# Performance work log

Measured on AMD Instinct MI355X. Metric: run time of the kernel, lower is better.

Reference implementation:

```python
import jax, jax.numpy as jnp
import numpy as np

N = 50000        # nodes
E = 800000       # edges (before self-loops)
F_IN = 128       # num_features
HID = 32         # hidden_size per head
HEADS = 4
CLS = 40         # num_classes
NEG_SLOPE = 0.2  # PyG GATConv default leaky_relu slope


def setup_inputs() -> dict:
    key = jax.random.key(0)
    ks = jax.random.split(key, 10)
    s = lambda k, sh: (jax.random.normal(k, sh, jnp.float32) * 0.05)
    x = jax.random.normal(ks[0], (N, F_IN), jnp.float32)
    edge_index = jax.random.randint(ks[1], (2, E), 0, N, dtype=jnp.int64)
    W1 = s(ks[2], (F_IN, HEADS * HID))
    att_src1 = s(ks[3], (HEADS, HID))
    att_dst1 = s(ks[4], (HEADS, HID))
    b1 = jnp.zeros((HEADS * HID,), jnp.float32)
    W2 = s(ks[5], (HEADS * HID, CLS))
    att_src2 = s(ks[6], (1, CLS))
    att_dst2 = s(ks[7], (1, CLS))
    b2 = jnp.zeros((CLS,), jnp.float32)
    return {"x": x, "edge_index": edge_index, "W1": W1, "att_src1": att_src1,
            "att_dst1": att_dst1, "b1": b1, "W2": W2, "att_src2": att_src2,
            "att_dst2": att_dst2, "b2": b2}


def _add_self_loops(edge_index, num_nodes):
    ar = jnp.arange(num_nodes, dtype=edge_index.dtype)
    loops = jnp.stack([ar, ar])
    return jnp.concatenate([edge_index, loops], axis=1)


def _gat_conv(x, edge_index, W, a_src, a_dst, bias, heads, concat):
    """PyG GATConv (eval mode, additive attention, self-loops already added)."""
    n = x.shape[0]
    src, dst = edge_index[0], edge_index[1]
    h = (x @ W).reshape(n, heads, -1)                 # [N, H, C]
    a_s = jnp.einsum('nhc,hc->nh', h, a_src)          # [N, H]
    a_d = jnp.einsum('nhc,hc->nh', h, a_dst)          # [N, H]
    e = jax.nn.leaky_relu(a_s[src] + a_d[dst], NEG_SLOPE)   # [E', H]
    m = jax.ops.segment_max(e, dst, num_segments=n)   # segment softmax over dst
    ex = jnp.exp(e - m[dst])
    den = jax.ops.segment_sum(ex, dst, num_segments=n)
    alpha = ex / den[dst]                             # [E', H]
    out = jax.ops.segment_sum(h[src] * alpha[:, :, None], dst, num_segments=n)
    out = out.reshape(n, -1) if concat else out.mean(axis=1)
    return out + bias


def reference(x, edge_index, W1, att_src1, att_dst1, b1, W2, att_src2, att_dst2, b2):
    ei = _add_self_loops(edge_index, x.shape[0])
    # dropout p=0 in eval -> identity
    h = jax.nn.relu(_gat_conv(x, ei, W1, att_src1, att_dst1, b1, HEADS, True))
    out = _gat_conv(h, ei, W2, att_src2, att_dst2, b2, 1, True)  # heads=1
    return out
```

## Files before the change

### kernel.cpp

```cpp
#include <hip/hip_runtime.h>
#include <cstdint>

#define NODES 50000
#define FIN   128
#define C1    128
#define HEADS 4
#define HID   32
#define CLS   40
#define SLOPE 0.2f

#define NBUCK ((NODES + 255) >> 8)
#define EPB 2048
#define BCAP 8192

__device__ __forceinline__ float lrelu(float v) { return v > 0.f ? v : SLOPE * v; }

__device__ __forceinline__ unsigned short f2bf(float f) {
    union { float f; unsigned u; } v; v.f = f;
    unsigned u = v.u;
    return (unsigned short)((u + 0x7FFFu + ((u >> 16) & 1u)) >> 16);
}
__device__ __forceinline__ float bf2f(unsigned short b) {
    union { unsigned u; float f; } v; v.u = ((unsigned)b) << 16;
    return v.f;
}
__device__ __forceinline__ float bflo(unsigned u) {
    union { unsigned x; float f; } v; v.x = u << 16; return v.f;
}
__device__ __forceinline__ float bfhi(unsigned u) {
    union { unsigned x; float f; } v; v.x = u & 0xffff0000u; return v.f;
}
__device__ __forceinline__ unsigned cvtpk(float a, float b) {
    unsigned r;
    asm("v_cvt_pk_bf16_f32 %0, %1, %2" : "=v"(r) : "v"(a), "v"(b));
    return r;
}

typedef __attribute__((ext_vector_type(8))) short bf16x8;
typedef __attribute__((ext_vector_type(4))) float f32x4;
typedef __attribute__((ext_vector_type(4), aligned(4))) int int4a;
typedef __attribute__((ext_vector_type(2), aligned(4))) int int2a;

__device__ __forceinline__ void acc8(float w, uint4 p, float* ac) {
    ac[0] = fmaf(w, bflo(p.x), ac[0]); ac[1] = fmaf(w, bfhi(p.x), ac[1]);
    ac[2] = fmaf(w, bflo(p.y), ac[2]); ac[3] = fmaf(w, bfhi(p.y), ac[3]);
    ac[4] = fmaf(w, bflo(p.z), ac[4]); ac[5] = fmaf(w, bfhi(p.z), ac[5]);
    ac[6] = fmaf(w, bflo(p.w), ac[6]); ac[7] = fmaf(w, bfhi(p.w), ac[7]);
}

__global__ __launch_bounds__(256) void k_prep(const float* __restrict__ W1,
                                              const float* __restrict__ W2,
                                              unsigned short* __restrict__ w1t,
                                              unsigned short* __restrict__ w2t,
                                              int* __restrict__ bwp) {
    const int b = blockIdx.x, t = threadIdx.x;
    if (b < 8) {
        __shared__ unsigned short Tb[16][136];
        const int n0 = b * 16;
        const int k = t & 127, g = t >> 7;
#pragma unroll
        for (int i = 0; i < 8; i++)
            Tb[g * 8 + i][k] = f2bf(W1[(size_t)k * C1 + n0 + g * 8 + i]);
        __syncthreads();
        {
            int nl = t >> 4, k8 = (t & 15) * 8;
            *(uint4*)(w1t + (n0 + nl) * 128 + k8) = *(uint4*)(&Tb[nl][k8]);
        }
    } else {
        for (int p = t; p < CLS * 128; p += 256) {
            int n = p >> 7, k = p & 127;
            w2t[n * 128 + k] = f2bf(W2[(size_t)k * CLS + n]);
        }
        if (t < NBUCK) bwp[t] = t * BCAP;
    }
}

__global__ __launch_bounds__(256) void k_front(const float* __restrict__ X,
                                               const unsigned short* __restrict__ w1t,
                                               const float* __restrict__ AS,
                                               const float* __restrict__ AD,
                                               unsigned short* __restrict__ h1b,
                                               float* __restrict__ as1,
                                               float* __restrict__ ad1,
                                               const int* __restrict__ src,
                                               const int* __restrict__ dst, int E,
                                               int* __restrict__ bwp,
                                               int* __restrict__ tmp, int GB1) {
    __shared__ unsigned short Asm[64][136];
    __shared__ unsigned short Wt[128][136];
    __shared__ int cnt[NBUCK];
    __shared__ int bbs[NBUCK];
    const int t = threadIdx.x;

    if (blockIdx.x >= GB1) {
        for (int i = t; i < NBUCK; i += 256) cnt[i] = 0;
        __syncthreads();
        const int e0 = (blockIdx.x - GB1) * EPB;
        int v[8], rb[8];
#pragma unroll
        for (int k = 0; k < 8; k++) {
            int e = e0 + k * 256 + t;
            rb[k] = -1;
            if (e < E) {
                int d = dst[e], s = src[e];
                int b = d >> 8;
                int r = atomicAdd(&cnt[b], 1);
                v[k] = (s << 8) | (d & 255);
                rb[k] = (r << 8) | b;
            }
        }
        __syncthreads();
        for (int i = t; i < NBUCK; i += 256) {
            int c = cnt[i];
            bbs[i] = c ? atomicAdd(&bwp[i], c) : 0;
        }
        __syncthreads();
#pragma unroll
        for (int k = 0; k < 8; k++) {
            if (rb[k] >= 0) {
                int b = rb[k] & 255;
                int r = rb[k] >> 8;
                tmp[bbs[b] + r] = v[k];
            }
        }
        return;
    }

    const int row0 = blockIdx.x * 64;
#pragma unroll
    for (int i = 0; i < 8; i++) {
        int p = i * 256 + t;
        int n = p >> 4, k8 = (p & 15) * 8;
        *(uint4*)(&Wt[n][k8]) = *(const uint4*)(w1t + n * 128 + k8);
    }
    {
        int r = t >> 2, c0 = (t & 3) * 32;
        int gr = row0 + r;
        if (gr < NODES) {
#pragma unroll
            for (int i = 0; i < 4; i++) {
                float4 va = *(const float4*)(X + (size_t)gr * FIN + c0 + i * 8);
                float4 vb = *(const float4*)(X + (size_t)gr * FIN + c0 + i * 8 + 4);
                uint4 pk;
                pk.x = cvtpk(va.x, va.y);
                pk.y = cvtpk(va.z, va.w);
                pk.z = cvtpk(vb.x, vb.y);
                pk.w = cvtpk(vb.z, vb.w);
                *(uint4*)(&Asm[r][c0 + i * 8]) = pk;
            }
        } else {
            uint4 z = make_uint4(0, 0, 0, 0);
#pragma unroll
            for (int i = 0; i < 4; i++) *(uint4*)(&Asm[r][c0 + i * 8]) = z;
        }
    }
    __syncthreads();

    const int w = t >> 6, l = t & 63;
    const int lm = l & 15, quad = l >> 4;
    f32x4 acc[8];
#pragma unroll
    for (int ct = 0; ct < 8; ct++) acc[ct] = (f32x4){0.f, 0.f, 0.f, 0.f};
#pragma unroll
    for (int kt = 0; kt < 4; kt++) {
        bf16x8 a = *(const bf16x8*)(&Asm[w * 16 + lm][kt * 32 + quad * 8]);
#pragma unroll
        for (int ct = 0; ct < 8; ct++) {
            bf16x8 b = *(const bf16x8*)(&Wt[ct * 16 + lm][kt * 32 + quad * 8]);
            acc[ct] = __builtin_amdgcn_mfma_f32_16x16x32_bf16(a, b, acc[ct], 0, 0, 0);
        }
    }
    __syncthreads();
#pragma unroll
    for (int ct = 0; ct < 8; ct++)
#pragma unroll
        for (int r = 0; r < 4; r++)
            Asm[w * 16 + quad * 4 + r][ct * 16 + lm] = f2bf(acc[ct][r]);
    __syncthreads();
    {
        int r = t >> 2, c0 = (t & 3) * 32;
        int gr = row0 + r;
        if (gr < NODES) {
#pragma unroll
            for (int i = 0; i < 4; i++)
                *(uint4*)(h1b + (size_t)gr * C1 + c0 + i * 8) =
                    *(uint4*)(&Asm[r][c0 + i * 8]);
        }
    }
    {
        int r = t >> 2, h = t & 3;
        int gr = row0 + r;
        if (gr < NODES) {
            float s = 0.f, d = 0.f;
#pragma unroll
            for (int i = 0; i < 4; i++) {
                uint4 hv = *(const uint4*)(&Asm[r][h * 32 + i * 8]);
                float4 a0 = *(const float4*)(AS + h * HID + i * 8);
                float4 a1 = *(const float4*)(AS + h * HID + i * 8 + 4);
                float4 d0 = *(const float4*)(AD + h * HID + i * 8);
                float4 d1 = *(const float4*)(AD + h * HID + i * 8 + 4);
                float v0 = bflo(hv.x), v1 = bfhi(hv.x), v2 = bflo(hv.y), v3 = bfhi(hv.y);
                float v4 = bflo(hv.z), v5 = bfhi(hv.z), v6 = bflo(hv.w), v7 = bfhi(hv.w);
                s = fmaf(v0, a0.x, s); s = fmaf(v1, a0.y, s);
                s = fmaf(v2, a0.z, s); s = fmaf(v3, a0.w, s);
                s = fmaf(v4, a1.x, s); s = fmaf(v5, a1.y, s);
                s = fmaf(v6, a1.z, s); s = fmaf(v7, a1.w, s);
                d = fmaf(v0, d0.x, d); d = fmaf(v1, d0.y, d);
                d = fmaf(v2, d0.z, d); d = fmaf(v3, d0.w, d);
                d = fmaf(v4, d1.x, d); d = fmaf(v5, d1.y, d);
                d = fmaf(v6, d1.z, d); d = fmaf(v7, d1.w, d);
            }
            as1[gr * HEADS + h] = s;
            ad1[gr * HEADS + h] = d;
        }
    }
}

__global__ __launch_bounds__(512) void k_bucketB(const int* __restrict__ bwp,
                                                 const int* __restrict__ tmp,
                                                 int* __restrict__ col,
                                                 int* __restrict__ rowptr,
                                                 int* __restrict__ degarr) {
    __shared__ int degs[256];
    __shared__ int wp[256];
    __shared__ int wsum[4];
    const int b = blockIdx.x, t = threadIdx.x;
    const int n0 = b << 8;
    const int beg = b * BCAP;
    const int end = bwp[b];
    if (t < 256) degs[t] = 0;
    __syncthreads();
    for (int e = beg + t; e < end; e += 512)
        atomicAdd(&degs[tmp[e] & 255], 1);
    __syncthreads();
    int d = 0, incl = 0;
    const int lane = t & 63, w = t >> 6;
    if (t < 256) {
        d = degs[t];
        incl = d;
#pragma unroll
        for (int s = 1; s < 64; s <<= 1) {
            int u = __shfl_up(incl, s);
            if (lane >= s) incl += u;
        }
        if (lane == 63) wsum[w] = incl;
    }
    __syncthreads();
    if (t == 0) {
        int r = 0;
#pragma unroll
        for (int i = 0; i < 4; i++) { int x = wsum[i]; wsum[i] = r; r += x; }
    }
    __syncthreads();
    if (t < 256) {
        const int excl = incl - d + wsum[w] + beg;
        const int nidx = n0 + t;
        if (nidx < NODES) { rowptr[nidx] = excl; degarr[nidx] = d; }
        wp[t] = excl;
    }
    __syncthreads();
    for (int e = beg + t; e < end; e += 512) {
        int v = tmp[e];
        int p = atomicAdd(&wp[v & 255], 1);
        col[p] = v >> 8;
    }
}

__global__ __launch_bounds__(256) void k_agg1(const unsigned short* __restrict__ h1b,
                                              const float* __restrict__ as1,
                                              const float* __restrict__ ad1,
                                              const int* __restrict__ rowptr,
                                              const int* __restrict__ degarr,
                                              const int* __restrict__ col,
                                              const float* __restrict__ b1,
                                              unsigned short* __restrict__ out1) {
    int wid = (blockIdx.x * 256 + threadIdx.x) >> 6;
    if (wid >= NODES) return;
    const int lane = threadIdx.x & 63;
    const int q  = lane >> 4;
    const int ll = lane & 15;
    const int fh = ll >> 2;
    const int n = wid;
    const float adn = ad1[n * HEADS + fh];
    const int rs = rowptr[n];
    const int re = rs + degarr[n];
    const unsigned lo = (unsigned)(ll << 4);

    float den = 0.f;
    float ac[8];
#pragma unroll
    for (int k = 0; k < 8; k++) ac[k] = 0.f;

    int base = rs;
    for (; re - base > 16; base += 32) {
        int4a ca = *(const int4a*)(col + base + q * 4);
        int4a cb = *(const int4a*)(col + base + 16 + q * 4);
        const int ia = base + q * 4;
        const int ib = base + 16 + q * 4;
        int c0 = (ia + 0 < re) ? ca.x : n;
        int c1 = (ia + 1 < re) ? ca.y : n;
        int c2 = (ia + 2 < re) ? ca.z : n;
        int c3 = (ia + 3 < re) ? ca.w : n;
        int c4 = (ib + 0 < re) ? cb.x : n;
        int c5 = (ib + 1 < re) ? cb.y : n;
        int c6 = (ib + 2 < re) ? cb.z : n;
        int c7 = (ib + 3 < re) ? cb.w : n;
        float w0 = __expf(lrelu(as1[c0 * HEADS + fh] + adn)); if (ia + 0 >= re) w0 = 0.f;
        float w1 = __expf(lrelu(as1[c1 * HEADS + fh] + adn)); if (ia + 1 >= re) w1 = 0.f;
        float w2 = __expf(lrelu(as1[c2 * HEADS + fh] + adn)); if (ia + 2 >= re) w2 = 0.f;
        float w3 = __expf(lrelu(as1[c3 * HEADS + fh] + adn)); if (ia + 3 >= re) w3 = 0.f;
        float w4 = __expf(lrelu(as1[c4 * HEADS + fh] + adn)); if (ib + 0 >= re) w4 = 0.f;
        float w5 = __expf(lrelu(as1[c5 * HEADS + fh] + adn)); if (ib + 1 >= re) w5 = 0.f;
        float w6 = __expf(lrelu(as1[c6 * HEADS + fh] + adn)); if (ib + 2 >= re) w6 = 0.f;
        float w7 = __expf(lrelu(as1[c7 * HEADS + fh] + adn)); if (ib + 3 >= re) w7 = 0.f;
        den += ((w0 + w1) + (w2 + w3)) + ((w4 + w5) + (w6 + w7));
        uint4 p0 = *(const uint4*)((const char*)h1b + (((unsigned)c0 << 8) + lo));
        uint4 p1 = *(const uint4*)((const char*)h1b + (((unsigned)c1 << 8) + lo));
        uint4 p2 = *(const uint4*)((const char*)h1b + (((unsigned)c2 << 8) + lo));
        uint4 p3 = *(const uint4*)((const char*)h1b + (((unsigned)c3 << 8) + lo));
        uint4 p4 = *(const uint4*)((const char*)h1b + (((unsigned)c4 << 8) + lo));
        uint4 p5 = *(const uint4*)((const char*)h1b + (((unsigned)c5 << 8) + lo));
        uint4 p6 = *(const uint4*)((const char*)h1b + (((unsigned)c6 << 8) + lo));
        uint4 p7 = *(const uint4*)((const char*)h1b + (((unsigned)c7 << 8) + lo));
        acc8(w0, p0, ac); acc8(w1, p1, ac); acc8(w2, p2, ac); acc8(w3, p3, ac);
        acc8(w4, p4, ac); acc8(w5, p5, ac); acc8(w6, p6, ac); acc8(w7, p7, ac);
    }
    if (base < re) {
        int4a ca = *(const int4a*)(col + base + q * 4);
        const int ia = base + q * 4;
        int c0 = (ia + 0 < re) ? ca.x : n;
        int c1 = (ia + 1 < re) ? ca.y : n;
        int c2 = (ia + 2 < re) ? ca.z : n;
        int c3 = (ia + 3 < re) ? ca.w : n;
        float w0 = __expf(lrelu(as1[c0 * HEADS + fh] + adn)); if (ia + 0 >= re) w0 = 0.f;
        float w1 = __expf(lrelu(as1[c1 * HEADS + fh] + adn)); if (ia + 1 >= re) w1 = 0.f;
        float w2 = __expf(lrelu(as1[c2 * HEADS + fh] + adn)); if (ia + 2 >= re) w2 = 0.f;
        float w3 = __expf(lrelu(as1[c3 * HEADS + fh] + adn)); if (ia + 3 >= re) w3 = 0.f;
        den += (w0 + w1) + (w2 + w3);
        uint4 p0 = *(const uint4*)((const char*)h1b + (((unsigned)c0 << 8) + lo));
        uint4 p1 = *(const uint4*)((const char*)h1b + (((unsigned)c1 << 8) + lo));
        uint4 p2 = *(const uint4*)((const char*)h1b + (((unsigned)c2 << 8) + lo));
        uint4 p3 = *(const uint4*)((const char*)h1b + (((unsigned)c3 << 8) + lo));
        acc8(w0, p0, ac); acc8(w1, p1, ac); acc8(w2, p2, ac); acc8(w3, p3, ac);
    }
    den += __shfl_xor(den, 16);
    den += __shfl_xor(den, 32);
#pragma unroll
    for (int k = 0; k < 8; k++) {
        ac[k] += __shfl_xor(ac[k], 16);
        ac[k] += __shfl_xor(ac[k], 32);
    }
    const float wself = __expf(lrelu(as1[n * HEADS + fh] + adn));
    den += wself;
    if (q == 0) {
        unsigned offs = ((unsigned)n << 8) + lo;
        uint4 sp = *(const uint4*)((const char*)h1b + offs);
        float sv[8] = {bflo(sp.x), bfhi(sp.x), bflo(sp.y), bfhi(sp.y),
                       bflo(sp.z), bfhi(sp.z), bflo(sp.w), bfhi(sp.w)};
        float4 bv0 = *(const float4*)(b1 + ll * 8);
        float4 bv1 = *(const float4*)(b1 + ll * 8 + 4);
        float bb[8] = {bv0.x, bv0.y, bv0.z, bv0.w, bv1.x, bv1.y, bv1.z, bv1.w};
        const float inv = 1.f / den;
        float o[8];
#pragma unroll
        for (int k = 0; k < 8; k++)
            o[k] = fmaxf(fmaf(wself, sv[k], ac[k]) * inv + bb[k], 0.f);
        uint4 pk;
        pk.x = cvtpk(o[0], o[1]);
        pk.y = cvtpk(o[2], o[3]);
        pk.z = cvtpk(o[4], o[5]);
        pk.w = cvtpk(o[6], o[7]);
        *(uint4*)(out1 + (size_t)n * C1 + ll * 8) = pk;
    }
}

__global__ __launch_bounds__(256) void k_gemm2(const unsigned short* __restrict__ out1b,
                                               const unsigned short* __restrict__ w2t,
                                               const float* __restrict__ AS,
                                               const float* __restrict__ AD,
                                               unsigned short* __restrict__ h2b,
                                               float* __restrict__ as2,
                                               float* __restrict__ ad2) {
    __shared__ unsigned short Asm[64][136];
    __shared__ unsigned short Wt2[48][136];
    __shared__ float Cc[64][52];
    const int t = threadIdx.x;
    const int row0 = blockIdx.x * 64;

    for (int p = t; p < 8 * 136; p += 256) Wt2[40 + p / 136][p % 136] = 0;
    for (int p = t; p < 640; p += 256) {
        int n = p >> 4, k8 = (p & 15) * 8;
        *(uint4*)(&Wt2[n][k8]) = *(const uint4*)(w2t + n * 128 + k8);
    }
    {
        int r = t >> 2, c0 = (t & 3) * 32;
        int gr = row0 + r;
        if (gr < NODES) {
#pragma unroll
            for (int i = 0; i < 4; i++)
                *(uint4*)(&Asm[r][c0 + i * 8]) =
                    *(const uint4*)(out1b + (size_t)gr * C1 + c0 + i * 8);
        } else {
            uint4 z = make_uint4(0, 0, 0, 0);
#pragma unroll
            for (int i = 0; i < 4; i++) *(uint4*)(&Asm[r][c0 + i * 8]) = z;
        }
    }
    __syncthreads();

    const int w = t >> 6, l = t & 63;
    const int lm = l & 15, quad = l >> 4;
    f32x4 acc[3];
#pragma unroll
    for (int ct = 0; ct < 3; ct++) acc[ct] = (f32x4){0.f, 0.f, 0.f, 0.f};
#pragma unroll
    for (int kt = 0; kt < 4; kt++) {
        bf16x8 a = *(const bf16x8*)(&Asm[w * 16 + lm][kt * 32 + quad * 8]);
#pragma unroll
        for (int ct = 0; ct < 3; ct++) {
            bf16x8 b = *(const bf16x8*)(&Wt2[ct * 16 + lm][kt * 32 + quad * 8]);
            acc[ct] = __builtin_amdgcn_mfma_f32_16x16x32_bf16(a, b, acc[ct], 0, 0, 0);
        }
    }
    __syncthreads();
#pragma unroll
    for (int ct = 0; ct < 3; ct++)
#pragma unroll
        for (int r = 0; r < 4; r++)
            Cc[w * 16 + quad * 4 + r][ct * 16 + lm] = acc[ct][r];
    __syncthreads();
    {
        int r = t >> 2, c0 = (t & 3) * 10;
        int gr = row0 + r;
        if (gr < NODES) {
#pragma unroll
            for (int i = 0; i < 5; i++) {
                int c = c0 + i * 2;
                unsigned pk = cvtpk(Cc[r][c], Cc[r][c + 1]);
                *(unsigned*)(h2b + (size_t)gr * 40 + c) = pk;
            }
            float s = 0.f, d = 0.f;
#pragma unroll
            for (int j = 0; j < 10; j++) {
                float v = Cc[r][c0 + j];
                s = fmaf(v, AS[c0 + j], s);
                d = fmaf(v, AD[c0 + j], d);
            }
            s += __shfl_xor(s, 1); s += __shfl_xor(s, 2);
            d += __shfl_xor(d, 1); d += __shfl_xor(d, 2);
            if ((t & 3) == 0) { as2[gr] = s; ad2[gr] = d; }
        }
    }
}

__global__ __launch_bounds__(256) void k_agg2(const unsigned short* __restrict__ h2b,
                                              const float* __restrict__ as2,
                                              const float* __restrict__ ad2,
                                              const int* __restrict__ rowptr,
                                              const int* __restrict__ degarr,
                                              const int* __restrict__ col,
                                              const float* __restrict__ b2,
                                              float* __restrict__ out) {
    int wid = (blockIdx.x * 256 + threadIdx.x) >> 6;
    if (wid >= NODES) return;
    const int lane = threadIdx.x & 63;
    const int q8 = lane >> 3, l8 = lane & 7;
    const int n = wid;
    const float adn = ad2[n];
    const int rs = rowptr[n];
    const int re = rs + degarr[n];
    const unsigned lo = (unsigned)(l8 << 4);

    float den = 0.f;
    float ac[8];
#pragma unroll
    for (int k = 0; k < 8; k++) ac[k] = 0.f;

    int base = rs;
    for (; re - base > 16; base += 32) {
        int4a cc = *(const int4a*)(col + base + q8 * 4);
        const int i0 = base + q8 * 4;
        int c0 = (i0 + 0 < re) ? cc.x : n;
        int c1 = (i0 + 1 < re) ? cc.y : n;
        int c2 = (i0 + 2 < re) ? cc.z : n;
        int c3 = (i0 + 3 < re) ? cc.w : n;
        float w0 = __expf(lrelu(as2[c0] + adn)); if (i0 + 0 >= re) w0 = 0.f;
        float w1 = __expf(lrelu(as2[c1] + adn)); if (i0 + 1 >= re) w1 = 0.f;
        float w2 = __expf(lrelu(as2[c2] + adn)); if (i0 + 2 >= re) w2 = 0.f;
        float w3 = __expf(lrelu(as2[c3] + adn)); if (i0 + 3 >= re) w3 = 0.f;
        den += (w0 + w1) + (w2 + w3);
        if (l8 < 5) {
            uint4 p0 = *(const uint4*)((const char*)h2b + ((unsigned)c0 * 80u + lo));
            uint4 p1 = *(const uint4*)((const char*)h2b + ((unsigned)c1 * 80u + lo));
            uint4 p2 = *(const uint4*)((const char*)h2b + ((unsigned)c2 * 80u + lo));
            uint4 p3 = *(const uint4*)((const char*)h2b + ((unsigned)c3 * 80u + lo));
            acc8(w0, p0, ac); acc8(w1, p1, ac);
            acc8(w2, p2, ac); acc8(w3, p3, ac);
        }
    }
    if (base < re) {
        int2a cc = *(const int2a*)(col + base + q8 * 2);
        const int i0 = base + q8 * 2;
        int c0 = (i0 + 0 < re) ? cc.x : n;
        int c1 = (i0 + 1 < re) ? cc.y : n;
        float w0 = __expf(lrelu(as2[c0] + adn)); if (i0 + 0 >= re) w0 = 0.f;
        float w1 = __expf(lrelu(as2[c1] + adn)); if (i0 + 1 >= re) w1 = 0.f;
        den += w0 + w1;
        if (l8 < 5) {
            uint4 p0 = *(const uint4*)((const char*)h2b + ((unsigned)c0 * 80u + lo));
            uint4 p1 = *(const uint4*)((const char*)h2b + ((unsigned)c1 * 80u + lo));
            acc8(w0, p0, ac); acc8(w1, p1, ac);
        }
    }
    den += __shfl_xor(den, 8);
    den += __shfl_xor(den, 16);
    den += __shfl_xor(den, 32);
#pragma unroll
    for (int k = 0; k < 8; k++) {
        ac[k] += __shfl_xor(ac[k], 8);
        ac[k] += __shfl_xor(ac[k], 16);
        ac[k] += __shfl_xor(ac[k], 32);
    }
    const float wself = __expf(lrelu(as2[n] + adn));
    den += wself;
    if (q8 == 0 && l8 < 5) {
        unsigned offs = (unsigned)n * 80u + lo;
        uint4 sp = *(const uint4*)((const char*)h2b + offs);
        float sv[8] = {bflo(sp.x), bfhi(sp.x), bflo(sp.y), bfhi(sp.y),
                       bflo(sp.z), bfhi(sp.z), bflo(sp.w), bfhi(sp.w)};
        float4 bv0 = *(const float4*)(b2 + l8 * 8);
        float4 bv1 = *(const float4*)(b2 + l8 * 8 + 4);
        float bb[8] = {bv0.x, bv0.y, bv0.z, bv0.w, bv1.x, bv1.y, bv1.z, bv1.w};
        float o[8];
#pragma unroll
        for (int k = 0; k < 8; k++)
            o[k] = (ac[k] + wself * sv[k]) / den + bb[k];
        *(float4*)(out + (size_t)n * CLS + l8 * 8) =
            make_float4(o[0], o[1], o[2], o[3]);
        *(float4*)(out + (size_t)n * CLS + l8 * 8 + 4) =
            make_float4(o[4], o[5], o[6], o[7]);
    }
}

extern "C" void kernel_launch(void* const* d_in, const int* in_sizes, int n_in,
                              void* d_out, int out_size, void* d_ws, size_t ws_size,
                              hipStream_t stream) {
    const float* x     = (const float*)d_in[0];
    const int*   ei    = (const int*)d_in[1];
    const float* W1    = (const float*)d_in[2];
    const float* aS1   = (const float*)d_in[3];
    const float* aD1   = (const float*)d_in[4];
    const float* b1    = (const float*)d_in[5];
    const float* W2    = (const float*)d_in[6];
    const float* aS2   = (const float*)d_in[7];
    const float* aD2   = (const float*)d_in[8];
    const float* b2    = (const float*)d_in[9];
    float* out = (float*)d_out;
    const int E = in_sizes[1] / 2;
    const int* src = ei;
    const int* dst = ei + E;

    char* ws = (char*)d_ws;
    size_t off = 0;
    auto alloc = [&](size_t bytes) -> char* {
        char* p = ws + off;
        off += (bytes + 255) & ~(size_t)255;
        return p;
    };
    unsigned short* h1b  = (unsigned short*)alloc((size_t)NODES * C1 * 2);
    unsigned short* out1 = (unsigned short*)alloc((size_t)NODES * C1 * 2);
    unsigned short* h2b  = (unsigned short*)alloc((size_t)NODES * 40 * 2);
    float* as1    = (float*)alloc((size_t)NODES * HEADS * 4);
    float* ad1    = (float*)alloc((size_t)NODES * HEADS * 4);
    float* as2    = (float*)alloc((size_t)NODES * 4);
    float* ad2    = (float*)alloc((size_t)NODES * 4);
    int* rowptr   = (int*)alloc((size_t)NODES * 4);
    int* degarr   = (int*)alloc((size_t)NODES * 4);
    int* col      = (int*)alloc((size_t)NBUCK * BCAP * 4 + 1024);
    int* tmp      = (int*)alloc((size_t)NBUCK * BCAP * 4 + 1024);
    unsigned short* w1t = (unsigned short*)alloc((size_t)FIN * C1 * 2);
    unsigned short* w2t = (unsigned short*)alloc((size_t)CLS * 128 * 2);
    int* bwp      = (int*)alloc((size_t)NBUCK * 4);

    const int GB1 = (NODES + 63) / 64;
    const int GBA = (E + EPB - 1) / EPB;

    k_prep<<<9, 256, 0, stream>>>(W1, W2, w1t, w2t, bwp);
    k_front<<<GB1 + GBA, 256, 0, stream>>>(x, w1t, aS1, aD1, h1b, as1, ad1,
                                           src, dst, E, bwp, tmp, GB1);
    k_bucketB<<<NBUCK, 512, 0, stream>>>(bwp, tmp, col, rowptr, degarr);
    k_agg1<<<(NODES * 64) / 256, 256, 0, stream>>>(h1b, as1, ad1, rowptr, degarr,
                                                   col, b1, out1);
    k_gemm2<<<(NODES + 63) / 64, 256, 0, stream>>>(out1, w2t, aS2, aD2, h2b, as2, ad2);
    k_agg2<<<(NODES * 64) / 256, 256, 0, stream>>>(h2b, as2, ad2, rowptr, degarr,
                                                   col, b2, out);
}
```

Measured before the change: 189.7 us.

## Count degrees with global atomics in front pass; process two row tiles per GEMM block

Per-node in-degree is now counted with global atomicAdd during edge bucketing in k_front (degarr zeroed by extra k_prep blocks), so k_bucketB no longer makes its first pass over tmp to build shared-memory histograms and instead reads the precomputed degrees. The GEMM part of k_front now handles two 64-row tiles per block, reusing the W1 tile staged in LDS and halving the number of GEMM blocks. In exchange it adds 800K scattered global atomics and more serialized work per GEMM block.

```diff
diff --git a/kernel.cpp b/kernel.cpp
--- a/kernel.cpp
+++ b/kernel.cpp
@@ -52,7 +52,8 @@
                                               const float* __restrict__ W2,
                                               unsigned short* __restrict__ w1t,
                                               unsigned short* __restrict__ w2t,
-                                              int* __restrict__ bwp) {
+                                              int* __restrict__ bwp,
+                                              int* __restrict__ degarr) {
     const int b = blockIdx.x, t = threadIdx.x;
     if (b < 8) {
         __shared__ unsigned short Tb[16][136];
@@ -66,12 +67,19 @@
             int nl = t >> 4, k8 = (t & 15) * 8;
             *(uint4*)(w1t + (n0 + nl) * 128 + k8) = *(uint4*)(&Tb[nl][k8]);
         }
-    } else {
+    } else if (b == 8) {
         for (int p = t; p < CLS * 128; p += 256) {
             int n = p >> 7, k = p & 127;
             w2t[n * 128 + k] = f2bf(W2[(size_t)k * CLS + n]);
         }
         if (t < NBUCK) bwp[t] = t * BCAP;
+    } else {
+        const int i0 = (b - 9) * 1024;
+#pragma unroll
+        for (int i = 0; i < 4; i++) {
+            int idx = i0 + i * 256 + t;
+            if (idx < NODES) degarr[idx] = 0;
+        }
     }
 }
 
@@ -85,7 +93,8 @@
                                                const int* __restrict__ src,
                                                const int* __restrict__ dst, int E,
                                                int* __restrict__ bwp,
-                                               int* __restrict__ tmp, int GB1) {
+                                               int* __restrict__ tmp,
+                                               int* __restrict__ degarr, int GB1) {
     __shared__ unsigned short Asm[64][136];
     __shared__ unsigned short Wt[128][136];
     __shared__ int cnt[NBUCK];
@@ -105,6 +114,7 @@
                 int d = dst[e], s = src[e];
                 int b = d >> 8;
                 int r = atomicAdd(&cnt[b], 1);
+                atomicAdd(&degarr[d], 1);
                 v[k] = (s << 8) | (d & 255);
                 rb[k] = (r << 8) | b;
             }
@@ -126,117 +136,117 @@
         return;
     }
 
-    const int row0 = blockIdx.x * 64;
+    const int tile0 = blockIdx.x * 128;
 #pragma unroll
     for (int i = 0; i < 8; i++) {
         int p = i * 256 + t;
         int n = p >> 4, k8 = (p & 15) * 8;
         *(uint4*)(&Wt[n][k8]) = *(const uint4*)(w1t + n * 128 + k8);
     }
-    {
-        int r = t >> 2, c0 = (t & 3) * 32;
-        int gr = row0 + r;
-        if (gr < NODES) {
-#pragma unroll
-            for (int i = 0; i < 4; i++) {
-                float4 va = *(const float4*)(X + (size_t)gr * FIN + c0 + i * 8);
-                float4 vb = *(const float4*)(X + (size_t)gr * FIN + c0 + i * 8 + 4);
-                uint4 pk;
-                pk.x = cvtpk(va.x, va.y);
-                pk.y = cvtpk(va.z, va.w);
-                pk.z = cvtpk(vb.x, vb.y);
-                pk.w = cvtpk(vb.z, vb.w);
-                *(uint4*)(&Asm[r][c0 + i * 8]) = pk;
-            }
-        } else {
-            uint4 z = make_uint4(0, 0, 0, 0);
-#pragma unroll
-            for (int i = 0; i < 4; i++) *(uint4*)(&Asm[r][c0 + i * 8]) = z;
-        }
-    }
-    __syncthreads();
-
     const int w = t >> 6, l = t & 63;
     const int lm = l & 15, quad = l >> 4;
-    f32x4 acc[8];
-#pragma unroll
-    for (int ct = 0; ct < 8; ct++) acc[ct] = (f32x4){0.f, 0.f, 0.f, 0.f};
-#pragma unroll
-    for (int kt = 0; kt < 4; kt++) {
-        bf16x8 a = *(const bf16x8*)(&Asm[w * 16 + lm][kt * 32 + quad * 8]);
-#pragma unroll
-        for (int ct = 0; ct < 8; ct++) {
-            bf16x8 b = *(const bf16x8*)(&Wt[ct * 16 + lm][kt * 32 + quad * 8]);
-            acc[ct] = __builtin_amdgcn_mfma_f32_16x16x32_bf16(a, b, acc[ct], 0, 0, 0);
-        }
-    }
-    __syncthreads();
-#pragma unroll
-    for (int ct = 0; ct < 8; ct++)
-#pragma unroll
-        for (int r = 0; r < 4; r++)
-            Asm[w * 16 + quad * 4 + r][ct * 16 + lm] = f2bf(acc[ct][r]);
-    __syncthreads();
-    {
-        int r = t >> 2, c0 = (t & 3) * 32;
-        int gr = row0 + r;
-        if (gr < NODES) {
-#pragma unroll
-            for (int i = 0; i < 4; i++)
-                *(uint4*)(h1b + (size_t)gr * C1 + c0 + i * 8) =
-                    *(uint4*)(&Asm[r][c0 + i * 8]);
-        }
-    }
-    {
-        int r = t >> 2, h = t & 3;
-        int gr = row0 + r;
-        if (gr < NODES) {
-            float s = 0.f, d = 0.f;
-#pragma unroll
-            for (int i = 0; i < 4; i++) {
-                uint4 hv = *(const uint4*)(&Asm[r][h * 32 + i * 8]);
-                float4 a0 = *(const float4*)(AS + h * HID + i * 8);
-                float4 a1 = *(const float4*)(AS + h * HID + i * 8 + 4);
-                float4 d0 = *(const float4*)(AD + h * HID + i * 8);
-                float4 d1 = *(const float4*)(AD + h * HID + i * 8 + 4);
-                float v0 = bflo(hv.x), v1 = bfhi(hv.x), v2 = bflo(hv.y), v3 = bfhi(hv.y);
-                float v4 = bflo(hv.z), v5 = bfhi(hv.z), v6 = bflo(hv.w), v7 = bfhi(hv.w);
-                s = fmaf(v0, a0.x, s); s = fmaf(v1, a0.y, s);
-                s = fmaf(v2, a0.z, s); s = fmaf(v3, a0.w, s);
-                s = fmaf(v4, a1.x, s); s = fmaf(v5, a1.y, s);
-                s = fmaf(v6, a1.z, s); s = fmaf(v7, a1.w, s);
-                d = fmaf(v0, d0.x, d); d = fmaf(v1, d0.y, d);
-                d = fmaf(v2, d0.z, d); d = fmaf(v3, d0.w, d);
-                d = fmaf(v4, d1.x, d); d = fmaf(v5, d1.y, d);
-                d = fmaf(v6, d1.z, d); d = fmaf(v7, d1.w, d);
-            }
-            as1[gr * HEADS + h] = s;
-            ad1[gr * HEADS + h] = d;
+#pragma unroll
+    for (int rt = 0; rt < 2; rt++) {
+        const int row0 = tile0 + rt * 64;
+        if (rt) __syncthreads();
+        {
+            int r = t >> 2, c0 = (t & 3) * 32;
+            int gr = row0 + r;
+            if (gr < NODES) {
+#pragma unroll
+                for (int i = 0; i < 4; i++) {
+                    float4 va = *(const float4*)(X + (size_t)gr * FIN + c0 + i * 8);
+                    float4 vb = *(const float4*)(X + (size_t)gr * FIN + c0 + i * 8 + 4);
+                    uint4 pk;
+                    pk.x = cvtpk(va.x, va.y);
+                    pk.y = cvtpk(va.z, va.w);
+                    pk.z = cvtpk(vb.x, vb.y);
+                    pk.w = cvtpk(vb.z, vb.w);
+                    *(uint4*)(&Asm[r][c0 + i * 8]) = pk;
+                }
+            } else {
+                uint4 z = make_uint4(0, 0, 0, 0);
+#pragma unroll
+                for (int i = 0; i < 4; i++) *(uint4*)(&Asm[r][c0 + i * 8]) = z;
+            }
+        }
+        __syncthreads();
+
+        f32x4 acc[8];
+#pragma unroll
+        for (int ct = 0; ct < 8; ct++) acc[ct] = (f32x4){0.f, 0.f, 0.f, 0.f};
+#pragma unroll
+        for (int kt = 0; kt < 4; kt++) {
+            bf16x8 a = *(const bf16x8*)(&Asm[w * 16 + lm][kt * 32 + quad * 8]);
+#pragma unroll
+            for (int ct = 0; ct < 8; ct++) {
+                bf16x8 b = *(const bf16x8*)(&Wt[ct * 16 + lm][kt * 32 + quad * 8]);
+                acc[ct] = __builtin_amdgcn_mfma_f32_16x16x32_bf16(a, b, acc[ct], 0, 0, 0);
+            }
+        }
+        __syncthreads();
+#pragma unroll
+        for (int ct = 0; ct < 8; ct++)
+#pragma unroll
+            for (int r = 0; r < 4; r++)
+                Asm[w * 16 + quad * 4 + r][ct * 16 + lm] = f2bf(acc[ct][r]);
+        __syncthreads();
+        {
+            int r = t >> 2, c0 = (t & 3) * 32;
+            int gr = row0 + r;
+            if (gr < NODES) {
+#pragma unroll
+                for (int i = 0; i < 4; i++)
+                    *(uint4*)(h1b + (size_t)gr * C1 + c0 + i * 8) =
+                        *(uint4*)(&Asm[r][c0 + i * 8]);
+            }
+        }
+        {
+            int r = t >> 2, h = t & 3;
+            int gr = row0 + r;
+            if (gr < NODES) {
+                float s = 0.f, d = 0.f;
+#pragma unroll
+                for (int i = 0; i < 4; i++) {
+                    uint4 hv = *(const uint4*)(&Asm[r][h * 32 + i * 8]);
+                    float4 a0 = *(const float4*)(AS + h * HID + i * 8);
+                    float4 a1 = *(const float4*)(AS + h * HID + i * 8 + 4);
+                    float4 d0 = *(const float4*)(AD + h * HID + i * 8);
+                    float4 d1 = *(const float4*)(AD + h * HID + i * 8 + 4);
+                    float v0 = bflo(hv.x), v1 = bfhi(hv.x), v2 = bflo(hv.y), v3 = bfhi(hv.y);
+                    float v4 = bflo(hv.z), v5 = bfhi(hv.z), v6 = bflo(hv.w), v7 = bfhi(hv.w);
+                    s = fmaf(v0, a0.x, s); s = fmaf(v1, a0.y, s);
+                    s = fmaf(v2, a0.z, s); s = fmaf(v3, a0.w, s);
+                    s = fmaf(v4, a1.x, s); s = fmaf(v5, a1.y, s);
+                    s = fmaf(v6, a1.z, s); s = fmaf(v7, a1.w, s);
+                    d = fmaf(v0, d0.x, d); d = fmaf(v1, d0.y, d);
+                    d = fmaf(v2, d0.z, d); d = fmaf(v3, d0.w, d);
+                    d = fmaf(v4, d1.x, d); d = fmaf(v5, d1.y, d);
+                    d = fmaf(v6, d1.z, d); d = fmaf(v7, d1.w, d);
+                }
+                as1[gr * HEADS + h] = s;
+                ad1[gr * HEADS + h] = d;
+            }
         }
     }
 }
 
 __global__ __launch_bounds__(512) void k_bucketB(const int* __restrict__ bwp,
                                                  const int* __restrict__ tmp,
+                                                 const int* __restrict__ degarr,
                                                  int* __restrict__ col,
-                                                 int* __restrict__ rowptr,
-                                                 int* __restrict__ degarr) {
-    __shared__ int degs[256];
+                                                 int* __restrict__ rowptr) {
     __shared__ int wp[256];
     __shared__ int wsum[4];
     const int b = blockIdx.x, t = threadIdx.x;
     const int n0 = b << 8;
     const int beg = b * BCAP;
     const int end = bwp[b];
-    if (t < 256) degs[t] = 0;
-    __syncthreads();
-    for (int e = beg + t; e < end; e += 512)
-        atomicAdd(&degs[tmp[e] & 255], 1);
-    __syncthreads();
     int d = 0, incl = 0;
     const int lane = t & 63, w = t >> 6;
     if (t < 256) {
-        d = degs[t];
+        const int nidx = n0 + t;
+        d = (nidx < NODES) ? degarr[nidx] : 0;
         incl = d;
 #pragma unroll
         for (int s = 1; s < 64; s <<= 1) {
@@ -255,7 +265,7 @@
     if (t < 256) {
         const int excl = incl - d + wsum[w] + beg;
         const int nidx = n0 + t;
-        if (nidx < NODES) { rowptr[nidx] = excl; degarr[nidx] = d; }
+        if (nidx < NODES) rowptr[nidx] = excl;
         wp[t] = excl;
     }
     __syncthreads();
@@ -582,13 +592,13 @@
     unsigned short* w2t = (unsigned short*)alloc((size_t)CLS * 128 * 2);
     int* bwp      = (int*)alloc((size_t)NBUCK * 4);
 
-    const int GB1 = (NODES + 63) / 64;
+    const int GB1 = (NODES + 127) / 128;
     const int GBA = (E + EPB - 1) / EPB;
 
-    k_prep<<<9, 256, 0, stream>>>(W1, W2, w1t, w2t, bwp);
+    k_prep<<<9 + (NODES + 1023) / 1024, 256, 0, stream>>>(W1, W2, w1t, w2t, bwp, degarr);
     k_front<<<GB1 + GBA, 256, 0, stream>>>(x, w1t, aS1, aD1, h1b, as1, ad1,
-                                           src, dst, E, bwp, tmp, GB1);
-    k_bucketB<<<NBUCK, 512, 0, stream>>>(bwp, tmp, col, rowptr, degarr);
+                                           src, dst, E, bwp, tmp, degarr, GB1);
+    k_bucketB<<<NBUCK, 512, 0, stream>>>(bwp, tmp, degarr, col, rowptr);
     k_agg1<<<(NODES * 64) / 256, 256, 0, stream>>>(h1b, as1, ad1, rowptr, degarr,
                                                    col, b1, out1);
     k_gemm2<<<(NODES + 63) / 64, 256, 0, stream>>>(out1, w2t, aS2, aD2, h2b, as2, ad2);
```

Result: slower. 211.0 us (+11.2%).
